# Kernel tuning notes

Measured on AMD Instinct MI355X. Metric: run time of the kernel, lower is better.

Reference implementation:

```python
import jax, jax.numpy as jnp
import numpy as np

COST_CLASS = 1.0
COST_BBOX = 1.0
COST_GIOU = 1.0


def box_cxcywh_to_xyxy(b):
    cx, cy, w, h = jnp.split(b, 4, axis=-1)
    return jnp.concatenate([cx - 0.5 * w, cy - 0.5 * h, cx + 0.5 * w, cy + 0.5 * h], axis=-1)


def generalized_box_iou(b1, b2):
    # b1: [N,4] xyxy, b2: [M,4] xyxy -> [N,M]
    a1 = (b1[:, 2] - b1[:, 0]) * (b1[:, 3] - b1[:, 1])  # [N]
    a2 = (b2[:, 2] - b2[:, 0]) * (b2[:, 3] - b2[:, 1])  # [M]
    lt = jnp.maximum(b1[:, None, :2], b2[None, :, :2])  # [N,M,2]
    rb = jnp.minimum(b1[:, None, 2:], b2[None, :, 2:])
    wh = jnp.clip(rb - lt, 0.0)
    inter = wh[..., 0] * wh[..., 1]
    union = a1[:, None] + a2[None, :] - inter
    iou = inter / union
    lt_e = jnp.minimum(b1[:, None, :2], b2[None, :, :2])
    rb_e = jnp.maximum(b1[:, None, 2:], b2[None, :, 2:])
    wh_e = jnp.clip(rb_e - lt_e, 0.0)
    area = wh_e[..., 0] * wh_e[..., 1]
    return iou - (area - union) / area


def setup_inputs() -> dict:
    key = jax.random.key(0)
    k1, k2, k3, k4, k5 = jax.random.split(key, 5)
    bs, nq, d, total_tgt = 16, 900, 256, 1600
    return {
        "pred_logits": jax.random.normal(k1, (bs, nq, d), dtype=jnp.float32),
        "pred_boxes": jax.random.uniform(k2, (bs, nq, 4), dtype=jnp.float32),
        "tgt_embs": jax.random.normal(k3, (total_tgt, d), dtype=jnp.float32),
        "tgt_bbox": jax.random.uniform(k4, (total_tgt, 4), dtype=jnp.float32),
        "tgt_sizes": jax.random.randint(k5, (bs,), 0, 100, dtype=jnp.int32),  # only used by host-side LSA
    }


def reference(pred_logits, pred_boxes, tgt_embs, tgt_bbox, tgt_sizes):
    # Returns the sigmoid-squashed cost volume C [bs, num_queries, total_tgt];
    # scipy linear_sum_assignment over tgt_sizes splits is a host-side step.
    bs, nq = pred_logits.shape[:2]
    out_prob = pred_logits.reshape(bs * nq, -1)
    out_bbox = pred_boxes.reshape(bs * nq, 4)
    out_prob = out_prob / jnp.linalg.norm(out_prob, axis=-1, keepdims=True)
    cost_class = jax.nn.relu(out_prob @ tgt_embs.T)                    # [N,M]
    cost_bbox = jnp.sum(jnp.abs(out_bbox[:, None, :] - tgt_bbox[None, :, :]), axis=-1)  # L1 cdist
    cost_giou = -generalized_box_iou(box_cxcywh_to_xyxy(out_bbox), box_cxcywh_to_xyxy(tgt_bbox))
    C = COST_BBOX * cost_bbox + COST_CLASS * cost_class + COST_GIOU * cost_giou
    return jax.nn.sigmoid(C.reshape(bs, nq, -1))
```

## Files before the change

### kernel.cpp

```cpp
#include <hip/hip_runtime.h>

#define N_ROWS 14400
#define M_COLS 1600
#define KDIM   256
#define GRID_X 25
#define GRID_Y 113
#define NWG    (GRID_X * GRID_Y)

typedef __attribute__((ext_vector_type(8))) short bf16x8;
typedef __attribute__((ext_vector_type(4))) float f32x4;

__device__ __forceinline__ short f2bf(float x) {
  union { float f; unsigned u; } v; v.f = x;
  unsigned r = v.u + 0x7FFFu + ((v.u >> 16) & 1u);
  return (short)(r >> 16);
}

__device__ __forceinline__ void gload_lds16(const void* g, void* l) {
  __builtin_amdgcn_global_load_lds(
      (const __attribute__((address_space(1))) void*)g,
      (__attribute__((address_space(3))) void*)l, 16, 0, 0);
}

__global__ __launch_bounds__(256) void prep_kernel(
    const float* __restrict__ logits, const float* __restrict__ embs,
    short* __restrict__ probB, short* __restrict__ embB) {
  const int row = blockIdx.x * 4 + (threadIdx.x >> 6);
  const int lane = threadIdx.x & 63;
  if (row < N_ROWS) {
    const float4 x = ((const float4*)(logits + (size_t)row * KDIM))[lane];
    float s = x.x * x.x + x.y * x.y + x.z * x.z + x.w * x.w;
#pragma unroll
    for (int o = 32; o > 0; o >>= 1) s += __shfl_xor(s, o, 64);
    const float scale = __builtin_amdgcn_rsqf(s);
    short4 o4;
    o4.x = f2bf(x.x * scale); o4.y = f2bf(x.y * scale);
    o4.z = f2bf(x.z * scale); o4.w = f2bf(x.w * scale);
    ((short4*)(probB + (size_t)row * KDIM))[lane] = o4;
  } else {
    const int r = row - N_ROWS;
    const float4 x = ((const float4*)(embs + (size_t)r * KDIM))[lane];
    short4 o4;
    o4.x = f2bf(x.x); o4.y = f2bf(x.y); o4.z = f2bf(x.z); o4.w = f2bf(x.w);
    ((short4*)(embB + (size_t)r * KDIM))[lane] = o4;
  }
}

__global__ __launch_bounds__(256) void cost_kernel(
    const short* __restrict__ probB, const short* __restrict__ embB,
    const float* __restrict__ pbox, const float* __restrict__ tbox,
    float* __restrict__ out) {
  __shared__ short As[128 * 64];
  __shared__ short Bs[64 * 64];
  __shared__ f32x4 rowcc[128], rowxy[128];
  __shared__ f32x4 colcc[64],  colxy[64];
  float* const tbuf = (float*)As;

  const int t = threadIdx.x;
  const int lane = t & 63;
  const int wid = t >> 6;
  const int wr = wid >> 1;
  const int wc = wid & 1;

  const int orig = blockIdx.x;
  const int xcd = orig & 7;
  const int rem = orig >> 3;
  const int q = NWG >> 3, r = NWG & 7;
  const int wgid = (xcd < r ? xcd * (q + 1) : r * (q + 1) + (xcd - r) * q) + rem;
  const int bx = wgid % GRID_X;
  const int by = wgid / GRID_X;
  const int rowBase = by * 128;
  const int colBase = bx * 64;

  if (t < 128) {
    const int idx = rowBase + t;
    const int ci = idx < N_ROWS ? idx : N_ROWS - 1;
    const float4 bb = ((const float4*)pbox)[ci];
    rowcc[t] = (f32x4){bb.x, bb.y, bb.z, bb.w};
    rowxy[t] = (f32x4){fmaf(-0.5f, bb.z, bb.x), fmaf(-0.5f, bb.w, bb.y),
                       fmaf(0.5f, bb.z, bb.x), fmaf(0.5f, bb.w, bb.y)};
  } else if (t < 192) {
    const int c = t - 128;
    const float4 bb = ((const float4*)tbox)[colBase + c];
    colcc[c] = (f32x4){bb.x, bb.y, bb.z, bb.w};
    colxy[c] = (f32x4){fmaf(-0.5f, bb.z, bb.x), fmaf(-0.5f, bb.w, bb.y),
                       fmaf(0.5f, bb.z, bb.x), fmaf(0.5f, bb.w, bb.y)};
  }

  f32x4 acc[4][2];
#pragma unroll
  for (int i = 0; i < 4; ++i)
#pragma unroll
    for (int j = 0; j < 2; ++j) acc[i][j] = (f32x4){0.f, 0.f, 0.f, 0.f};

  const int swz = (lane & 7) ^ (lane >> 3);
  const int rbase = wid * 8 + (lane >> 3);

  for (int kt = 0; kt < 4; ++kt) {
    const int k0 = kt * 64 + swz * 8;
#pragma unroll
    for (int i = 0; i < 4; ++i) {
      int gr = rowBase + i * 32 + rbase;
      if (gr > N_ROWS - 1) gr = N_ROWS - 1;
      gload_lds16(probB + (size_t)gr * KDIM + k0, As + (i * 32 + wid * 8) * 64);
    }
#pragma unroll
    for (int i = 0; i < 2; ++i) {
      const int gc = colBase + i * 32 + rbase;
      gload_lds16(embB + (size_t)gc * KDIM + k0, Bs + (i * 32 + wid * 8) * 64);
    }
    __syncthreads();
#pragma unroll
    for (int kk = 0; kk < 2; ++kk) {
      bf16x8 af[4], bfr[2];
      const int g = kk * 4 + (lane >> 4);
#pragma unroll
      for (int mi = 0; mi < 4; ++mi) {
        const int row = wr * 64 + mi * 16 + (lane & 15);
        af[mi] = *(const bf16x8*)(As + row * 64 + ((g ^ (row & 7)) * 8));
      }
#pragma unroll
      for (int ni = 0; ni < 2; ++ni) {
        const int row = wc * 32 + ni * 16 + (lane & 15);
        bfr[ni] = *(const bf16x8*)(Bs + row * 64 + ((g ^ (row & 7)) * 8));
      }
#pragma unroll
      for (int mi = 0; mi < 4; ++mi)
#pragma unroll
        for (int ni = 0; ni < 2; ++ni)
          acc[mi][ni] = __builtin_amdgcn_mfma_f32_16x16x32_bf16(
              af[mi], bfr[ni], acc[mi][ni], 0, 0, 0);
    }
    __syncthreads();
  }

  const float LOG2E = 1.44269504f;
  const int jr = (lane >> 4) * 4;
  const int lc = lane & 15;
  f32x4 c0v[2], c1v[2];
  float cav[2];
#pragma unroll
  for (int ni = 0; ni < 2; ++ni) {
    const int cloc = wc * 32 + ni * 16 + lc;
    c0v[ni] = colcc[cloc];
    c1v[ni] = colxy[cloc];
    cav[ni] = c0v[ni][2] * c0v[ni][3];
  }

#pragma unroll
  for (int mi = 0; mi < 4; ++mi) {
    float* const tb = tbuf + (mi & 1) * 2176;
#pragma unroll
    for (int j = 0; j < 4; ++j) {
      const int rloc = wr * 64 + mi * 16 + jr + j;
      const f32x4 r0 = rowcc[rloc];
      const f32x4 r1 = rowxy[rloc];
      const float ra = r0[2] * r0[3];
#pragma unroll
      for (int ni = 0; ni < 2; ++ni) {
        const f32x4 c0 = c0v[ni], c1 = c1v[ni];
        const float cc = fmaxf(acc[mi][ni][j], 0.0f);
        const float l1 = fabsf(r0[0] - c0[0]) + fabsf(r0[1] - c0[1]) +
                         fabsf(r0[2] - c0[2]) + fabsf(r0[3] - c0[3]);
        const float ltx = fmaxf(r1[0], c1[0]);
        const float lty = fmaxf(r1[1], c1[1]);
        const float rbx = fminf(r1[2], c1[2]);
        const float rby = fminf(r1[3], c1[3]);
        const float iw = fmaxf(rbx - ltx, 0.f);
        const float ih = fmaxf(rby - lty, 0.f);
        const float inter = iw * ih;
        const float uni = ra + cav[ni] - inter;
        const float ex = fmaxf(r1[2], c1[2]) - fminf(r1[0], c1[0]);
        const float ey = fmaxf(r1[3], c1[3]) - fminf(r1[1], c1[1]);
        const float earea = ex * ey;
        const float num = fmaf(uni, uni, inter * earea);
        const float Cv = l1 + cc + 1.0f
                         - num * __builtin_amdgcn_rcpf(uni * earea);
        const float sg = __builtin_amdgcn_rcpf(
            1.0f + __builtin_amdgcn_exp2f(-LOG2E * Cv));
        tb[(wr * 16 + jr + j) * 68 + wc * 32 + ni * 16 + lc] = sg;
      }
    }
    asm volatile("s_waitcnt lgkmcnt(0)" ::: "memory");
    __builtin_amdgcn_s_barrier();
#pragma unroll
    for (int rr = 0; rr < 2; ++rr) {
      const int rch = rr * 16 + (t >> 4);
      const int c4 = (t & 15) * 4;
      const f32x4 v = *(const f32x4*)(tb + rch * 68 + c4);
      const int grow = rowBase + ((rch < 16) ? (mi * 16 + rch)
                                             : (64 + mi * 16 + (rch - 16)));
      if (grow < N_ROWS)
        __builtin_nontemporal_store(
            v, (f32x4*)(out + (size_t)grow * M_COLS + colBase + c4));
    }
  }
}

extern "C" void kernel_launch(void* const* d_in, const int* in_sizes, int n_in,
                              void* d_out, int out_size, void* d_ws, size_t ws_size,
                              hipStream_t stream) {
  const float* logits = (const float*)d_in[0];
  const float* pbox   = (const float*)d_in[1];
  const float* embs   = (const float*)d_in[2];
  const float* tbox   = (const float*)d_in[3];
  float* out = (float*)d_out;

  short* probB = (short*)d_ws;
  short* embB  = probB + (size_t)N_ROWS * KDIM;

  prep_kernel<<<(N_ROWS + M_COLS) / 4, 256, 0, stream>>>(logits, embs, probB, embB);

  cost_kernel<<<NWG, 256, 0, stream>>>(probB, embB, pbox, tbox, out);
}
```

Before: 48.82 us.

## Double-buffer the GEMM K-loop with 32-wide K tiles in LDS

```diff
diff --git a/kernel.cpp b/kernel.cpp
--- a/kernel.cpp
+++ b/kernel.cpp
@@ -50,11 +50,11 @@
     const short* __restrict__ probB, const short* __restrict__ embB,
     const float* __restrict__ pbox, const float* __restrict__ tbox,
     float* __restrict__ out) {
-  __shared__ short As[128 * 64];
-  __shared__ short Bs[64 * 64];
+  __shared__ short As2[2][128 * 32];
+  __shared__ short Bs2[2][64 * 32];
   __shared__ f32x4 rowcc[128], rowxy[128];
   __shared__ f32x4 colcc[64],  colxy[64];
-  float* const tbuf = (float*)As;
+  float* const tbuf = (float*)As2;
 
   const int t = threadIdx.x;
   const int lane = t & 63;
@@ -93,44 +93,47 @@
 #pragma unroll
     for (int j = 0; j < 2; ++j) acc[i][j] = (f32x4){0.f, 0.f, 0.f, 0.f};
 
-  const int swz = (lane & 7) ^ (lane >> 3);
-  const int rbase = wid * 8 + (lane >> 3);
-
-  for (int kt = 0; kt < 4; ++kt) {
-    const int k0 = kt * 64 + swz * 8;
-#pragma unroll
-    for (int i = 0; i < 4; ++i) {
-      int gr = rowBase + i * 32 + rbase;
-      if (gr > N_ROWS - 1) gr = N_ROWS - 1;
-      gload_lds16(probB + (size_t)gr * KDIM + k0, As + (i * 32 + wid * 8) * 64);
-    }
-#pragma unroll
-    for (int i = 0; i < 2; ++i) {
-      const int gc = colBase + i * 32 + rbase;
-      gload_lds16(embB + (size_t)gc * KDIM + k0, Bs + (i * 32 + wid * 8) * 64);
-    }
-    __syncthreads();
-#pragma unroll
-    for (int kk = 0; kk < 2; ++kk) {
-      bf16x8 af[4], bfr[2];
-      const int g = kk * 4 + (lane >> 4);
-#pragma unroll
-      for (int mi = 0; mi < 4; ++mi) {
-        const int row = wr * 64 + mi * 16 + (lane & 15);
-        af[mi] = *(const bf16x8*)(As + row * 64 + ((g ^ (row & 7)) * 8));
-      }
-#pragma unroll
-      for (int ni = 0; ni < 2; ++ni) {
-        const int row = wc * 32 + ni * 16 + (lane & 15);
-        bfr[ni] = *(const bf16x8*)(Bs + row * 64 + ((g ^ (row & 7)) * 8));
-      }
-#pragma unroll
-      for (int mi = 0; mi < 4; ++mi)
-#pragma unroll
-        for (int ni = 0; ni < 2; ++ni)
-          acc[mi][ni] = __builtin_amdgcn_mfma_f32_16x16x32_bf16(
-              af[mi], bfr[ni], acc[mi][ni], 0, 0, 0);
-    }
+  const int srow = t >> 2;
+  const int sgran = (t & 3) ^ ((t >> 3) & 3);
+  const int adest = wid * 16 * 32;
+
+  int garow0 = rowBase + srow;        if (garow0 > N_ROWS - 1) garow0 = N_ROWS - 1;
+  int garow1 = rowBase + 64 + srow;   if (garow1 > N_ROWS - 1) garow1 = N_ROWS - 1;
+  const int gbrow = colBase + srow;
+
+#define STAGE(kt_, buf_)                                                      \
+  {                                                                           \
+    const int k0_ = (kt_)*32 + sgran * 8;                                     \
+    gload_lds16(probB + (size_t)garow0 * KDIM + k0_, &As2[buf_][adest]);      \
+    gload_lds16(probB + (size_t)garow1 * KDIM + k0_,                          \
+                &As2[buf_][64 * 32 + adest]);                                 \
+    gload_lds16(embB + (size_t)gbrow * KDIM + k0_, &Bs2[buf_][adest]);        \
+  }
+
+  STAGE(0, 0)
+  __syncthreads();
+
+  const int slot = (lane >> 4) ^ ((lane >> 1) & 3);
+  const int arow = wr * 64 + (lane & 15);
+  const int brow = wc * 32 + (lane & 15);
+
+#pragma unroll
+  for (int kt = 0; kt < 8; ++kt) {
+    const int buf = kt & 1;
+    if (kt < 7) STAGE(kt + 1, (kt + 1) & 1)
+    bf16x8 af[4], bfr[2];
+#pragma unroll
+    for (int mi = 0; mi < 4; ++mi)
+      af[mi] = *(const bf16x8*)(&As2[buf][(arow + mi * 16) * 32 + slot * 8]);
+#pragma unroll
+    for (int ni = 0; ni < 2; ++ni)
+      bfr[ni] = *(const bf16x8*)(&Bs2[buf][(brow + ni * 16) * 32 + slot * 8]);
+#pragma unroll
+    for (int mi = 0; mi < 4; ++mi)
+#pragma unroll
+      for (int ni = 0; ni < 2; ++ni)
+        acc[mi][ni] = __builtin_amdgcn_mfma_f32_16x16x32_bf16(
+            af[mi], bfr[ni], acc[mi][ni], 0, 0, 0);
     __syncthreads();
   }
 
@@ -195,6 +198,7 @@
             v, (f32x4*)(out + (size_t)grow * M_COLS + colBase + c4));
     }
   }
+#undef STAGE
 }
 
 extern "C" void kernel_launch(void* const* d_in, const int* in_sizes, int n_in,
```

Result: slower. 52.70 us (+7.9%).
